# Kernel tuning notes

Hardware: AMD Instinct MI355X
Metric: run time of the kernel (lower is better)

The kernel has to match this reference:

```python
import jax, jax.numpy as jnp
import numpy as np

DSIZE = 1024
STRIDES = [8, 16, 32]
FSIZES = [(128, 128), (64, 64), (32, 32)]
LAYOUTS = [[16, 32], [64, 128], [256, 512]]
IOU_THR = 0.3
B, M = 16, 128


def _gen_anchors():
    # replicates BBoxAnchors.generate_anchors: anchors in (cx, cy, w, h)
    outs = []
    for stride, (fw, fh), layout in zip(STRIDES, FSIZES, LAYOUTS):
        lay = np.array([[0.0, 0.0, float(w), float(w)] for w in layout], dtype=np.float32)  # [k,4]
        vx = np.arange(0.5, fw, dtype=np.float32) * stride
        vy = np.arange(0.5, fh, dtype=np.float32) * stride
        gy, gx = np.meshgrid(vy, vx, indexing='ij')
        off = np.stack([gx, gy], axis=-1)  # [fh,fw,2]
        a = np.broadcast_to(lay, (fh, fw, len(layout), 4)).copy()
        a[..., :2] += off[:, :, None, :]
        outs.append(a.reshape(-1, 4))
    return np.concatenate(outs, axis=0)  # [A,4]


def cbox2bbox(c):
    return jnp.concatenate([c[..., :2] - c[..., 2:] * 0.5, c[..., :2] + c[..., 2:] * 0.5], axis=-1)


def box_iou_pairwise(a, b):
    # a: [A,4] xyxy, b: [M,4] xyxy -> [A,M]
    lt = jnp.maximum(a[:, None, :2], b[None, :, :2])
    rb = jnp.minimum(a[:, None, 2:], b[None, :, 2:])
    wh = jnp.clip(rb - lt, 0.0)
    inter = wh[..., 0] * wh[..., 1]
    area_a = (a[:, 2] - a[:, 0]) * (a[:, 3] - a[:, 1])
    area_b = (b[:, 2] - b[:, 0]) * (b[:, 3] - b[:, 1])
    return inter / (area_a[:, None] + area_b[None, :] - inter)


def _match(banchors, labels, bboxes):
    iou = box_iou_pairwise(banchors, bboxes)  # [A,M]
    max_iou_of_anchor = iou.max(axis=1)
    box_indice = iou.argmax(axis=1)
    max_iou_of_bbox = iou.max(axis=0)
    anchor_indice = iou.argmax(axis=0)

    def body(carry, xs):
        mioa, bi = carry
        j, a, v = xs
        return (mioa.at[a].set(v), bi.at[a].set(j)), None

    (max_iou_of_anchor, box_indice), _ = jax.lax.scan(
        body, (max_iou_of_anchor, box_indice),
        (jnp.arange(M, dtype=box_indice.dtype), anchor_indice, max_iou_of_bbox))

    denom = jnp.maximum(max_iou_of_bbox, IOU_THR)[box_indice]
    max_iou_of_anchor = jnp.where(max_iou_of_anchor < IOU_THR * 0.5, 0.0, max_iou_of_anchor)
    scores = max_iou_of_anchor / denom
    scores = jnp.where(labels[box_indice] <= 0, 0.0, scores)
    return scores, box_indice


def setup_inputs() -> dict:
    key = jax.random.key(0)
    k1, k2, k3 = jax.random.split(key, 3)
    labels = jax.random.randint(k1, (B, M), 0, 5, dtype=jnp.int32)
    cxy = jax.random.uniform(k2, (B, M, 2), dtype=jnp.float32) * DSIZE
    wh = jax.random.uniform(k3, (B, M, 2), dtype=jnp.float32) * 248.0 + 8.0
    bboxes = jnp.concatenate([cxy - wh * 0.5, cxy + wh * 0.5], axis=-1)  # xyxy
    anchors = jnp.asarray(_gen_anchors())  # [43008,4] cxcywh
    return {"labels": labels, "bboxes": bboxes, "anchors": anchors}


def reference(labels, bboxes, anchors):
    banchors = cbox2bbox(anchors)  # [A,4]
    scores, bi = jax.vmap(lambda l, b: _match(banchors, l, b))(labels, bboxes)  # [B,A],[B,A]
    matched = jnp.take_along_axis(bboxes, bi[..., None], axis=1)  # [B,A,4]
    return scores, matched
```

## Files before the change

kernel.cpp:

```cpp
#include <hip/hip_runtime.h>
#include <stdint.h>

typedef unsigned long long u64;

#define A_TOTAL 43008
#define NB 16
#define NM 128
#define SPLIT 168
#define WPB 4

__device__ __forceinline__ float exact_div(float x, float y) {
    float r;
    asm("v_rcp_f32 %0, %1" : "=v"(r) : "v"(y));
    float e  = __builtin_fmaf(-y, r, 1.0f);
    r        = __builtin_fmaf(e, r, r);
    e        = __builtin_fmaf(-y, r, 1.0f);
    r        = __builtin_fmaf(e, r, r);
    float q  = x * r;
    float rs = __builtin_fmaf(-y, q, x);
    return __builtin_fmaf(rs, r, q);
}

__device__ __forceinline__ u64 dpp_u64(u64 v, const int ctrl) {
    int lo = (int)(unsigned)v, hi = (int)(unsigned)(v >> 32);
    int plo, phi;
    switch (ctrl) {
        case 0xB1:
            plo = __builtin_amdgcn_update_dpp(lo, lo, 0xB1, 0xF, 0xF, false);
            phi = __builtin_amdgcn_update_dpp(hi, hi, 0xB1, 0xF, 0xF, false);
            break;
        case 0x4E:
            plo = __builtin_amdgcn_update_dpp(lo, lo, 0x4E, 0xF, 0xF, false);
            phi = __builtin_amdgcn_update_dpp(hi, hi, 0x4E, 0xF, 0xF, false);
            break;
        default:
            plo = __builtin_amdgcn_update_dpp(lo, lo, 0x141, 0xF, 0xF, false);
            phi = __builtin_amdgcn_update_dpp(hi, hi, 0x141, 0xF, 0xF, false);
            break;
    }
    return ((u64)(unsigned)phi << 32) | (unsigned)plo;
}

__global__ __launch_bounds__(256) void prep_kernel(
    const float4* __restrict__ bboxes, float* __restrict__ areaBp,
    u64* __restrict__ colfinal, float4* __restrict__ chunkbnd) {
#pragma clang fp contract(off)
    const int i = blockIdx.x * 256 + threadIdx.x;
    float4 v = bboxes[i];
    areaBp[i] = (v.z - v.x) * (v.w - v.y);
    colfinal[i] = 0ull;
    if (blockIdx.x == 0) {
        const int t = threadIdx.x;
        const int base = (t >> 4) * NM + (t & 15) * 8;
        float4 f = bboxes[base];
        float mnx = f.x, mny = f.y, mxx = f.z, mxy = f.w;
#pragma unroll
        for (int k = 1; k < 8; ++k) {
            float4 u = bboxes[base + k];
            mnx = fminf(mnx, u.x); mny = fminf(mny, u.y);
            mxx = fmaxf(mxx, u.z); mxy = fmaxf(mxy, u.w);
        }
        chunkbnd[t] = make_float4(mnx, mny, mxx, mxy);
    }
}

__global__ __launch_bounds__(256) void fused_kernel(
    const float4* __restrict__ anchors, const float4* __restrict__ bbv,
    const float* __restrict__ areaBp, const float4* __restrict__ chunkbnd,
    u64* __restrict__ rowkey,
    u64* __restrict__ colfinal) {
#pragma clang fp contract(off)
    const int b = blockIdx.y, tid = threadIdx.x;
    const int lane = tid & 63, wv = tid >> 6;
    const int bi = lane >> 3, part = lane & 7;
    const int rbase = part * 8;

    __shared__ float s_col[WPB][8][65];

    const int w = blockIdx.x + wv * SPLIT;
    const int abase = w * 64;

    float4 an = anchors[abase + lane];
    float hw = an.z * 0.5f, hh = an.w * 0.5f;
    float ax1 = an.x - hw, ay1 = an.y - hh;
    float ax2 = an.x + hw, ay2 = an.y + hh;
    float areaA = (ax2 - ax1) * (ay2 - ay1);

    const float4* box  = bbv + (size_t)b * NM;
    const float*  area = areaBp + (size_t)b * NM;
    const float4* cb   = chunkbnd + (b << 4);

    unsigned cmask = 0;
#pragma unroll
    for (int c = 0; c < 16; ++c) {
        float4 gb = cb[c];
        bool cl = (gb.z > ax1) & (gb.x < ax2) & (gb.w > ay1) & (gb.y < ay2);
        if (__ballot(cl) != 0ull) cmask |= 1u << c;
    }

    float best_v = 0.0f; int best_m = 0;

    while (cmask) {
        const int c = __builtin_ctz(cmask);
        cmask &= cmask - 1;

        unsigned mask = 0;
#pragma unroll
        for (int i = 0; i < 8; ++i) {
            const int m = c * 8 + i;
            const float4 bx = box[m];
            bool lv = (bx.z > ax1) & (bx.x < ax2) & (bx.w > ay1) & (bx.y < ay2);
            if (__ballot(lv) != 0ull) {
                mask |= 1u << i;
                const float areaB = area[m];
                float ltx = fmaxf(ax1, bx.x), lty = fmaxf(ay1, bx.y);
                float rbx = fminf(ax2, bx.z), rby = fminf(ay2, bx.w);
                float wx = fmaxf(rbx - ltx, 0.0f), wy = fmaxf(rby - lty, 0.0f);
                float inter = wx * wy;
                float iou = exact_div(inter, (areaA + areaB) - inter);
                if (iou > best_v) { best_v = iou; best_m = m; }
                s_col[wv][i][lane] = iou;
            }
        }
        if (mask == 0u) continue;

        u64 key = 0ull;
        if (mask & (1u << bi)) {
            float v = -1.0f; int tb = 0;
#pragma unroll
            for (int t = 0; t < 8; ++t) {
                float o = s_col[wv][bi][rbase + t];
                if (o > v) { v = o; tb = t; }
            }
            unsigned aidx = (unsigned)(abase + rbase + tb);
            key = ((u64)__float_as_uint(v) << 32) | (u64)(unsigned)(~aidx);
        }
        { u64 o = dpp_u64(key, 0xB1);  if (o > key) key = o; }
        { u64 o = dpp_u64(key, 0x4E);  if (o > key) key = o; }
        { u64 o = dpp_u64(key, 0x141); if (o > key) key = o; }
        if (part == 0 && key)
            atomicMax(&colfinal[b * NM + c * 8 + bi], key);
    }

    rowkey[(size_t)b * A_TOTAL + abase + lane] =
        ((u64)__float_as_uint(best_v) << 32) | (u64)(unsigned)best_m;
}

__global__ __launch_bounds__(256) void epilogue_kernel(
    const float4* __restrict__ bboxes, const int* __restrict__ labels,
    const u64* __restrict__ colfinal, const u64* __restrict__ rowkey,
    float* __restrict__ out_scores, float4* __restrict__ out_matched) {
#pragma clang fp contract(off)
    const int b = blockIdx.y, tid = threadIdx.x;
    const int a0 = blockIdx.x * 256, a = a0 + tid;

    __shared__ float4 sbox[NM];
    __shared__ float  s_cm[NM];
    __shared__ int    s_lab[NM];
    __shared__ int    ovr[256];
    ovr[tid] = -1;

    int my_ca = -1;
    if (tid < NM) {
        u64 k = colfinal[b * NM + tid];
        s_cm[tid] = __uint_as_float((unsigned)(k >> 32));
        my_ca = ~((int)(unsigned)(k & 0xFFFFFFFFull));
        sbox[tid]  = bboxes[b * NM + tid];
        s_lab[tid] = labels[b * NM + tid];
    }
    __syncthreads();
    if (tid < NM && my_ca >= a0 && my_ca < a0 + 256)
        atomicMax(&ovr[my_ca - a0], tid);
    __syncthreads();

    u64 rk = rowkey[(size_t)b * A_TOTAL + a];
    float best = __uint_as_float((unsigned)(rk >> 32));
    int   bi   = (int)(rk & 0xFFFFFFFFull);

    int o = ovr[tid];
    if (o >= 0) { bi = o; best = s_cm[o]; }

    float denom = fmaxf(s_cm[bi], 0.3f);
    float val   = (best < 0.15f) ? 0.0f : best;
    float score = val / denom;
    if (s_lab[bi] <= 0) score = 0.0f;

    out_scores[(size_t)b * A_TOTAL + a]  = score;
    out_matched[(size_t)b * A_TOTAL + a] = sbox[bi];
}

extern "C" void kernel_launch(void* const* d_in, const int* in_sizes, int n_in,
                              void* d_out, int out_size, void* d_ws, size_t ws_size,
                              hipStream_t stream) {
    const int*    labels  = (const int*)d_in[0];
    const float4* bboxes  = (const float4*)d_in[1];
    const float4* anchors = (const float4*)d_in[2];

    float* out = (float*)d_out;

    char* ws = (char*)d_ws;
    u64*    rowkey   = (u64*)ws;                     ws += (size_t)NB * A_TOTAL * 8;
    u64*    colfinal = (u64*)ws;                     ws += (size_t)NB * NM * 8;
    float*  areaBp   = (float*)ws;                   ws += (size_t)NB * NM * 4;
    float4* chunkbnd = (float4*)ws;

    prep_kernel<<<(NB * NM) / 256, 256, 0, stream>>>(bboxes, areaBp, colfinal,
                                                     chunkbnd);

    dim3 g(SPLIT, NB);
    fused_kernel<<<g, 256, 0, stream>>>(anchors, bboxes, areaBp, chunkbnd,
                                        rowkey, colfinal);
    epilogue_kernel<<<g, 256, 0, stream>>>(
        bboxes, labels, colfinal, rowkey,
        out, (float4*)(out + (size_t)NB * A_TOTAL));
}
```

Measured before the change: 109.4 us.

## Rebalance anchor work by splitting large-anchor waves across GT chunks

The fused matching kernel now assigns work per anchor-wave type. The last 32 waves hold the largest anchors, which overlap many GT chunks, so each is split across four wavefronts that each handle four chunks. Their row maxima are merged in shared memory, with the index complemented so ties resolve to the lowest box index. Mid-size waves and the small-anchor waves are remapped to new block indices, and the grid grows from 168 to 192 blocks per batch. The aim is to reduce load imbalance from blocks that hold heavy large-anchor waves, at the cost of more blocks and an extra barrier and merge for the split units.

```diff
diff --git a/kernel.cpp b/kernel.cpp
--- a/kernel.cpp
+++ b/kernel.cpp
@@ -8,6 +8,7 @@
 #define NM 128
 #define SPLIT 168
 #define WPB 4
+#define FBLK 192
 
 __device__ __forceinline__ float exact_div(float x, float y) {
     float r;
@@ -64,20 +65,14 @@
     }
 }
 
-__global__ __launch_bounds__(256) void fused_kernel(
-    const float4* __restrict__ anchors, const float4* __restrict__ bbv,
-    const float* __restrict__ areaBp, const float4* __restrict__ chunkbnd,
-    u64* __restrict__ rowkey,
-    u64* __restrict__ colfinal) {
-#pragma clang fp contract(off)
-    const int b = blockIdx.y, tid = threadIdx.x;
-    const int lane = tid & 63, wv = tid >> 6;
+template<int CN>
+__device__ __forceinline__ u64 do_unit(
+    const int w, const int c0, const int b, const int lane,
+    const float4* __restrict__ anchors, const float4* __restrict__ box,
+    const float* __restrict__ area, const float4* __restrict__ cb,
+    float (*s_colw)[65], u64* __restrict__ colfinal) {
     const int bi = lane >> 3, part = lane & 7;
     const int rbase = part * 8;
-
-    __shared__ float s_col[WPB][8][65];
-
-    const int w = blockIdx.x + wv * SPLIT;
     const int abase = w * 64;
 
     float4 an = anchors[abase + lane];
@@ -86,23 +81,20 @@
     float ax2 = an.x + hw, ay2 = an.y + hh;
     float areaA = (ax2 - ax1) * (ay2 - ay1);
 
-    const float4* box  = bbv + (size_t)b * NM;
-    const float*  area = areaBp + (size_t)b * NM;
-    const float4* cb   = chunkbnd + (b << 4);
-
     unsigned cmask = 0;
 #pragma unroll
-    for (int c = 0; c < 16; ++c) {
-        float4 gb = cb[c];
+    for (int j = 0; j < CN; ++j) {
+        float4 gb = cb[c0 + j];
         bool cl = (gb.z > ax1) & (gb.x < ax2) & (gb.w > ay1) & (gb.y < ay2);
-        if (__ballot(cl) != 0ull) cmask |= 1u << c;
+        if (__ballot(cl) != 0ull) cmask |= 1u << j;
     }
 
     float best_v = 0.0f; int best_m = 0;
 
     while (cmask) {
-        const int c = __builtin_ctz(cmask);
+        const int j = __builtin_ctz(cmask);
         cmask &= cmask - 1;
+        const int c = c0 + j;
 
         unsigned mask = 0;
 #pragma unroll
@@ -119,7 +111,7 @@
                 float inter = wx * wy;
                 float iou = exact_div(inter, (areaA + areaB) - inter);
                 if (iou > best_v) { best_v = iou; best_m = m; }
-                s_col[wv][i][lane] = iou;
+                s_colw[i][lane] = iou;
             }
         }
         if (mask == 0u) continue;
@@ -129,7 +121,7 @@
             float v = -1.0f; int tb = 0;
 #pragma unroll
             for (int t = 0; t < 8; ++t) {
-                float o = s_col[wv][bi][rbase + t];
+                float o = s_colw[bi][rbase + t];
                 if (o > v) { v = o; tb = t; }
             }
             unsigned aidx = (unsigned)(abase + rbase + tb);
@@ -141,9 +133,52 @@
         if (part == 0 && key)
             atomicMax(&colfinal[b * NM + c * 8 + bi], key);
     }
-
-    rowkey[(size_t)b * A_TOTAL + abase + lane] =
-        ((u64)__float_as_uint(best_v) << 32) | (u64)(unsigned)best_m;
+    return ((u64)__float_as_uint(best_v) << 32) | (u64)(unsigned)(~best_m);
+}
+
+__global__ __launch_bounds__(256) void fused_kernel(
+    const float4* __restrict__ anchors, const float4* __restrict__ bbv,
+    const float* __restrict__ areaBp, const float4* __restrict__ chunkbnd,
+    u64* __restrict__ rowkey,
+    u64* __restrict__ colfinal) {
+#pragma clang fp contract(off)
+    const int b = blockIdx.y, x = blockIdx.x, tid = threadIdx.x;
+    const int lane = tid & 63, wv = tid >> 6;
+
+    __shared__ float s_col[WPB][8][65];
+    __shared__ u64   s_rk[WPB][64];
+
+    const float4* box  = bbv + (size_t)b * NM;
+    const float*  area = areaBp + (size_t)b * NM;
+    const float4* cb   = chunkbnd + (b << 4);
+    u64* rowb = rowkey + (size_t)b * A_TOTAL;
+
+    if (x < 32) {
+        const int w = 640 + x;
+        u64 mk = do_unit<4>(w, wv * 4, b, lane, anchors, box, area, cb,
+                            s_col[wv], colfinal);
+        s_rk[wv][lane] = mk;
+        __syncthreads();
+        if (wv == 0) {
+            u64 k = s_rk[0][lane];
+#pragma unroll
+            for (int t = 1; t < WPB; ++t) if (s_rk[t][lane] > k) k = s_rk[t][lane];
+            rowb[w * 64 + lane] =
+                (k & 0xFFFFFFFF00000000ull) | (u64)(unsigned)(~(unsigned)k);
+        }
+    } else if (x < 64) {
+        const int w = 512 + (x - 32) + wv * 32;
+        u64 mk = do_unit<16>(w, 0, b, lane, anchors, box, area, cb,
+                             s_col[wv], colfinal);
+        rowb[w * 64 + lane] =
+            (mk & 0xFFFFFFFF00000000ull) | (u64)(unsigned)(~(unsigned)mk);
+    } else {
+        const int w = (x - 64) + wv * 128;
+        u64 mk = do_unit<16>(w, 0, b, lane, anchors, box, area, cb,
+                             s_col[wv], colfinal);
+        rowb[w * 64 + lane] =
+            (mk & 0xFFFFFFFF00000000ull) | (u64)(unsigned)(~(unsigned)mk);
+    }
 }
 
 __global__ __launch_bounds__(256) void epilogue_kernel(
@@ -207,9 +242,10 @@
     prep_kernel<<<(NB * NM) / 256, 256, 0, stream>>>(bboxes, areaBp, colfinal,
                                                      chunkbnd);
 
+    fused_kernel<<<dim3(FBLK, NB), 256, 0, stream>>>(
+        anchors, bboxes, areaBp, chunkbnd, rowkey, colfinal);
+
     dim3 g(SPLIT, NB);
-    fused_kernel<<<g, 256, 0, stream>>>(anchors, bboxes, areaBp, chunkbnd,
-                                        rowkey, colfinal);
     epilogue_kernel<<<g, 256, 0, stream>>>(
         bboxes, labels, colfinal, rowkey,
         out, (float4*)(out + (size_t)NB * A_TOTAL));
```

New measurement: 111.5 us. No clear change (+1.8%).
